# Kernel tuning notes

Measured on AMD Instinct MI355X. Metric: run time of the kernel, lower is better.

Reference implementation:

```python
import jax, jax.numpy as jnp
import numpy as np

B, T, C = 4, 2048, 1024
H, D = 16, 64  # num_heads, head_size


def setup_inputs() -> dict:
    key = jax.random.key(0)
    ks = jax.random.split(key, 5)
    s = 0.02
    x = jax.random.normal(ks[0], (B, T, C), dtype=jnp.float32)
    Wq = jax.random.normal(ks[1], (H, C, D), dtype=jnp.float32) * s
    Wk = jax.random.normal(ks[2], (H, C, D), dtype=jnp.float32) * s
    Wv = jax.random.normal(ks[3], (H, C, D), dtype=jnp.float32) * s
    Wp = jax.random.normal(ks[4], (C, H * D), dtype=jnp.float32) * s  # Linear(H*D, C) weight
    bp = jnp.zeros((C,), dtype=jnp.float32)
    return {"x": x, "Wq": Wq, "Wk": Wk, "Wv": Wv, "Wp": Wp, "bp": bp}


def reference(x, Wq, Wk, Wv, Wp, bp):
    # per-head projections (all heads batched): [B,T,C] x [H,C,D] -> [B,H,T,D]
    q = jnp.einsum('btc,hcd->bhtd', x, Wq)
    k = jnp.einsum('btc,hcd->bhtd', x, Wk)
    v = jnp.einsum('btc,hcd->bhtd', x, Wv)
    scale = 1.0 / jnp.sqrt(jnp.asarray(D, dtype=x.dtype))
    scores = jnp.einsum('bhtd,bhsd->bhts', q, k) * scale  # [B,H,T,T]
    causal = jnp.tril(jnp.ones((T, T), dtype=bool))
    scores = jnp.where(causal, scores, -jnp.inf)
    w = jax.nn.softmax(scores, axis=-1)
    out = jnp.einsum('bhts,bhsd->bhtd', w, v)  # [B,H,T,D]
    out = out.transpose(0, 2, 1, 3).reshape(B, T, H * D)  # concat heads
    return out @ Wp.T + bp  # projection (dropout is identity in eval)
```

## Files before the change

kernel.cpp:

```cpp
#include <hip/hip_runtime.h>
#include <stdint.h>


typedef unsigned short u16;
typedef __attribute__((ext_vector_type(8))) short    s16x8;
typedef __attribute__((ext_vector_type(4))) float    f32x4;
typedef __attribute__((ext_vector_type(2))) uint32_t u32x2;


__device__ __forceinline__ u16 f2b(float f) {
  union { float f; uint32_t u; } v; v.f = f;
  uint32_t r = v.u + 0x7FFFu + ((v.u >> 16) & 1u);
  return (u16)(r >> 16);
}

__device__ __forceinline__ uint32_t cvtpk(float a, float b) {
  uint32_t r;
  asm("v_cvt_pk_bf16_f32 %0, %1, %2" : "=v"(r) : "v"(a), "v"(b));
  return r;
}

__device__ __forceinline__ f32x4 mfma_bf16(s16x8 a, s16x8 b, f32x4 c) {
  asm("v_mfma_f32_16x16x32_bf16 %0, %1, %2, %0" : "+v"(c) : "v"(a), "v"(b));
  return c;
}

__device__ __forceinline__ void gload_lds16(const void* g, void* l) {
  __builtin_amdgcn_global_load_lds(
      (__attribute__((address_space(1))) void*)(uintptr_t)g,
      (__attribute__((address_space(3))) void*)(uint32_t)(uintptr_t)l,
      16, 0, 0);
}


__global__ void cvt_f32_bf16_kernel(const float* __restrict__ in, u16* __restrict__ out) {
  size_t i = (size_t)blockIdx.x * 256 + threadIdx.x;
  const f32x4* p = (const f32x4*)(in + i * 8);
  f32x4 a = p[0], b = p[1];
  s16x8 o;
  o[0]=(short)f2b(a[0]); o[1]=(short)f2b(a[1]); o[2]=(short)f2b(a[2]); o[3]=(short)f2b(a[3]);
  o[4]=(short)f2b(b[0]); o[5]=(short)f2b(b[1]); o[6]=(short)f2b(b[2]); o[7]=(short)f2b(b[3]);
  *(s16x8*)(out + i * 8) = o;
}

__global__ void cvt_wqkv_kernel(const float* __restrict__ Wq, const float* __restrict__ Wk,
                                const float* __restrict__ Wv, u16* __restrict__ out) {
  int idx = blockIdx.x * 256 + threadIdx.x;
  int sel = idx >> 20;
  int rem = idx & 1048575;
  int n = rem >> 10, c = rem & 1023;
  int h = n >> 6, d = n & 63;
  const float* W = (sel == 0) ? Wq : ((sel == 1) ? Wk : Wv);
  out[idx] = f2b(W[h * 65536 + c * 64 + d]);
}


template <bool OUT_F32, bool BIAS>
__global__ __launch_bounds__(256) void gemm_bt_kernel(
    const u16* __restrict__ A, const u16* __restrict__ B, void* __restrict__ Cout,
    const float* __restrict__ bias, int K, int ldc)
{
  __shared__ __attribute__((aligned(16))) u16 As[128 * 64];
  __shared__ __attribute__((aligned(16))) u16 Bs[128 * 64];

  const int tid  = threadIdx.x;
  const int lane = tid & 63;
  const int w    = tid >> 6;
  const int wm   = w >> 1, wn = w & 1;
  const int g    = lane >> 4;
  const int li   = lane & 15;
  const size_t bm = (size_t)blockIdx.x * 128;
  const size_t bn = (size_t)blockIdx.y * 128;

  f32x4 acc[4][4] = {};

  const int kIters = K >> 6;
  for (int kt = 0; kt < kIters; ++kt) {
    const int kb = kt * 64;
#pragma unroll
    for (int i = 0; i < 4; ++i) {
      int c = i * 256 + tid;
      int row = c >> 3, sl = c & 7;
      int ss = sl ^ (row & 7);
      gload_lds16(A + (bm + row) * K + kb + ss * 8, &As[c * 8]);
      gload_lds16(B + (bn + row) * K + kb + ss * 8, &Bs[c * 8]);
    }
    __syncthreads();
#pragma unroll
    for (int ks = 0; ks < 2; ++ks) {
      s16x8 af[4], bfr[4];
#pragma unroll
      for (int f = 0; f < 4; ++f) {
        int ra = wm * 64 + f * 16 + li;
        int sa = (ks * 4 + g) ^ (ra & 7);
        af[f] = *(const s16x8*)&As[ra * 64 + sa * 8];
        int rb = wn * 64 + f * 16 + li;
        int sb = (ks * 4 + g) ^ (rb & 7);
        bfr[f] = *(const s16x8*)&Bs[rb * 64 + sb * 8];
      }
#pragma unroll
      for (int mi = 0; mi < 4; ++mi)
#pragma unroll
        for (int ni = 0; ni < 4; ++ni)
          acc[mi][ni] = mfma_bf16(af[mi], bfr[ni], acc[mi][ni]);
    }
    __syncthreads();
  }

#pragma unroll
  for (int ni = 0; ni < 4; ++ni) {
    size_t col = bn + wn * 64 + ni * 16 + li;
    float bv = BIAS ? bias[col] : 0.f;
#pragma unroll
    for (int mi = 0; mi < 4; ++mi) {
#pragma unroll
      for (int r = 0; r < 4; ++r) {
        size_t row = bm + wm * 64 + mi * 16 + g * 4 + r;
        if constexpr (OUT_F32) ((float*)Cout)[row * ldc + col] = acc[mi][ni][r] + bv;
        else                   ((u16*)Cout)[row * ldc + col] = f2b(acc[mi][ni][r]);
      }
    }
  }
}


__global__ __launch_bounds__(256) void transpose_v_kernel(const u16* __restrict__ qkv,
                                                          u16* __restrict__ vT) {
  __shared__ __attribute__((aligned(16))) u16 ts[64][72];
  const int bh = blockIdx.y;
  const int b = bh >> 4, h = bh & 15;
  const int t0 = blockIdx.x * 64;
  const u16* src = qkv + (size_t)(b * 2048 + t0) * 3072 + 2048 + h * 64;
#pragma unroll
  for (int i = 0; i < 2; ++i) {
    int c = i * 256 + threadIdx.x;
    int row = c >> 3, sl = c & 7;
    *(s16x8*)&ts[row][sl * 8] = *(const s16x8*)&src[(size_t)row * 3072 + sl * 8];
  }
  __syncthreads();
  u16* dst = vT + (size_t)bh * 64 * 2048 + t0;
#pragma unroll
  for (int i = 0; i < 2; ++i) {
    int c = i * 256 + threadIdx.x;
    int drow = c >> 3, sl = c & 7;
    s16x8 o;
#pragma unroll
    for (int j = 0; j < 8; ++j) o[j] = (short)ts[sl * 8 + j][drow];
    *(s16x8*)&dst[(size_t)drow * 2048 + sl * 8] = o;
  }
}


__global__ __launch_bounds__(256) void attn_kernel(const u16* __restrict__ qkv,
                                                   const u16* __restrict__ vT,
                                                   u16* __restrict__ out) {
  __shared__ __attribute__((aligned(16))) u16 Ks[2][64 * 64];
  __shared__ __attribute__((aligned(16))) u16 Vs[2][64 * 64];
  __shared__ __attribute__((aligned(16))) u16 Ps[4][16 * 64];

  const int id  = blockIdx.x;
  const int xcd = id & 7;
  const int rr  = id >> 3;
  const int bh  = xcd * 8 + (rr & 7);
  const int p   = rr >> 3;

  const int b = bh >> 4, h = bh & 15;
  const int tid = threadIdx.x;
  const int lane = tid & 63;
  const int w = tid >> 6;
  const int g = lane >> 4, li = lane & 15;

  const int tA = 31 - p;
  const int nA = tA + 1;
  const int nTot = nA + p + 1;

  const u16* kbase = qkv + (size_t)(b * 2048) * 3072 + 1024 + h * 64;
  const u16* vtb   = vT + (size_t)bh * 64 * 2048;
  u16* pl = Ps[w];

  auto stage = [&](int buf, int j0) {
#pragma unroll
    for (int i = 0; i < 2; ++i) {
      int c = i * 256 + tid;
      int row = c >> 3, sl = c & 7, ss = sl ^ (row & 7);
      gload_lds16(kbase + (size_t)(j0 + row) * 3072 + ss * 8, &Ks[buf][c * 8]);
      gload_lds16(vtb + (size_t)row * 2048 + j0 + ss * 8, &Vs[buf][c * 8]);
    }
  };

  stage(0, 0);
  __syncthreads();

  s16x8 qf[2];
  f32x4 oacc[4];
  float mrow = -1e30f, lrow = 0.f;
  int wq0 = 0, qglob = 0;
  const float cexp = 0.18033688011112042f;

  for (int s = 0; s < nTot; ++s) {
    const int cur = s & 1;
    const bool inA = s < nA;
    const int t  = inA ? s : s - nA;
    const int qt = inA ? tA : p;
    const int j0 = t * 64;

    if (s + 1 < nTot) {
      int t1 = (s + 1 < nA) ? (s + 1) : (s + 1 - nA);
      stage(cur ^ 1, t1 * 64);
    }

    if (t == 0) {
      wq0 = qt * 64 + w * 16;
      qglob = wq0 + li;
      const u16* qbase = qkv + (size_t)(b * 2048 + qglob) * 3072 + h * 64;
#pragma unroll
      for (int kk = 0; kk < 2; ++kk)
        qf[kk] = *(const s16x8*)&qbase[kk * 32 + g * 8];
      mrow = -1e30f; lrow = 0.f;
#pragma unroll
      for (int fd = 0; fd < 4; ++fd) oacc[fd] = (f32x4)0.f;
    }

    const u16* ksb = Ks[cur];
    const u16* vsb = Vs[cur];

    f32x4 sfr[4] = {};
#pragma unroll
    for (int kk = 0; kk < 2; ++kk) {
      s16x8 kf[4];
#pragma unroll
      for (int fj = 0; fj < 4; ++fj) {
        int rk = fj * 16 + li;
        int ssl = (kk * 4 + g) ^ (rk & 7);
        kf[fj] = *(const s16x8*)&ksb[rk * 64 + ssl * 8];
      }
#pragma unroll
      for (int fj = 0; fj < 4; ++fj)
        sfr[fj] = mfma_bf16(kf[fj], qf[kk], sfr[fj]);
    }

    if (t == qt) {
#pragma unroll
      for (int fj = 0; fj < 4; ++fj)
#pragma unroll
        for (int r = 0; r < 4; ++r) {
          int jj = j0 + fj * 16 + g * 4 + r;
          if (jj > qglob) sfr[fj][r] = -1e30f;
        }
    }

    float mx = sfr[0][0];
#pragma unroll
    for (int fj = 0; fj < 4; ++fj)
#pragma unroll
      for (int r = 0; r < 4; ++r) mx = fmaxf(mx, sfr[fj][r]);
    mx = fmaxf(mx, __shfl_xor(mx, 16));
    mx = fmaxf(mx, __shfl_xor(mx, 32));

    bool need = (mx - mrow) * cexp > 8.0f;
    if (__any(need)) {
      float mnew = fmaxf(mrow, mx);
      float sc = exp2f((mrow - mnew) * cexp);
      mrow = mnew;
      lrow *= sc;
#pragma unroll
      for (int fd = 0; fd < 4; ++fd)
#pragma unroll
        for (int r = 0; r < 4; ++r) oacc[fd][r] *= sc;
    }

    float rs = 0.f;
    const int lsw = li & 14;
#pragma unroll
    for (int fj = 0; fj < 4; ++fj) {
      float p0 = exp2f((sfr[fj][0] - mrow) * cexp);
      float p1 = exp2f((sfr[fj][1] - mrow) * cexp);
      float p2 = exp2f((sfr[fj][2] - mrow) * cexp);
      float p3 = exp2f((sfr[fj][3] - mrow) * cexp);
      rs += (p0 + p1) + (p2 + p3);
      u32x2 wv = { cvtpk(p0, p1), cvtpk(p2, p3) };
      int phys = (4 * fj + g) ^ lsw;
      *(u32x2*)&pl[li * 64 + phys * 4] = wv;
    }
    rs += __shfl_xor(rs, 16);
    rs += __shfl_xor(rs, 32);
    lrow += rs;

#pragma unroll
    for (int kk = 0; kk < 2; ++kk) {
      int sr = (8 * kk + 2 * g) ^ lsw;
      s16x8 pf = *(const s16x8*)&pl[li * 64 + sr * 4];
      s16x8 vf[4];
#pragma unroll
      for (int fd = 0; fd < 4; ++fd) {
        int rv = fd * 16 + li;
        int ssl = (kk * 4 + g) ^ (rv & 7);
        vf[fd] = *(const s16x8*)&vsb[rv * 64 + ssl * 8];
      }
#pragma unroll
      for (int fd = 0; fd < 4; ++fd)
        oacc[fd] = mfma_bf16(vf[fd], pf, oacc[fd]);
    }

    if (t == qt) {
      float inv = 1.f / lrow;
      u16* ob = out + (size_t)(b * 2048 + qglob) * 1024 + h * 64;
#pragma unroll
      for (int fd = 0; fd < 4; ++fd) {
        u32x2 wv = { cvtpk(oacc[fd][0] * inv, oacc[fd][1] * inv),
                     cvtpk(oacc[fd][2] * inv, oacc[fd][3] * inv) };
        *(u32x2*)&ob[fd * 16 + g * 4] = wv;
      }
    }

    __syncthreads();
  }
}


extern "C" void kernel_launch(void* const* d_in, const int* in_sizes, int n_in,
                              void* d_out, int out_size, void* d_ws, size_t ws_size,
                              hipStream_t stream) {
  const float* x  = (const float*)d_in[0];
  const float* Wq = (const float*)d_in[1];
  const float* Wk = (const float*)d_in[2];
  const float* Wv = (const float*)d_in[3];
  const float* Wp = (const float*)d_in[4];
  const float* bp = (const float*)d_in[5];
  (void)in_sizes; (void)n_in; (void)out_size; (void)ws_size;

  char* ws = (char*)d_ws;
  u16* xb    = (u16*)(ws);
  u16* wqkvb = (u16*)(ws + 16777216);
  u16* wpb   = (u16*)(ws + 23068672);
  u16* qkv   = (u16*)(ws + 25165824);
  u16* vT    = (u16*)(ws + 75497472);
  u16* ao    = (u16*)(ws + 92274688);

  cvt_f32_bf16_kernel<<<4096, 256, 0, stream>>>(x, xb);
  cvt_wqkv_kernel<<<12288, 256, 0, stream>>>(Wq, Wk, Wv, wqkvb);
  cvt_f32_bf16_kernel<<<512, 256, 0, stream>>>(Wp, wpb);

  gemm_bt_kernel<false, false><<<dim3(64, 24), 256, 0, stream>>>(
      xb, wqkvb, (void*)qkv, nullptr, 1024, 3072);

  transpose_v_kernel<<<dim3(32, 64), 256, 0, stream>>>(qkv, vT);

  attn_kernel<<<1024, 256, 0, stream>>>(qkv, vT, ao);

  gemm_bt_kernel<true, true><<<dim3(64, 8), 256, 0, stream>>>(
      ao, wpb, d_out, bp, 1024, 1024);
}
```

Before: 182.2 us.

## Fuse V transpose into QKV GEMM epilogue and precompute attention LDS offsets

The QKV GEMM epilogue now writes V columns directly in transposed [B,H,D,T] layout with packed bf16 stores, removing the separate transpose kernel and its extra read/write pass over V. The attention kernel precomputes swizzled LDS fragment offsets and simplifies K/V staging address math. It also raises wave priority around the MFMA sections with s_setprio and adds a min-blocks launch bound to help occupancy. The transposed stores are strided 8-byte writes, which may be less coalesced than the old transpose kernel's output.

```diff
diff --git a/kernel.cpp b/kernel.cpp
--- a/kernel.cpp
+++ b/kernel.cpp
@@ -55,10 +55,10 @@
 }
 
 
-template <bool OUT_F32, bool BIAS>
+template <int MODE>
 __global__ __launch_bounds__(256) void gemm_bt_kernel(
     const u16* __restrict__ A, const u16* __restrict__ B, void* __restrict__ Cout,
-    const float* __restrict__ bias, int K, int ldc)
+    const float* __restrict__ bias, u16* __restrict__ vTout, int K, int ldc)
 {
   __shared__ __attribute__((aligned(16))) u16 As[128 * 64];
   __shared__ __attribute__((aligned(16))) u16 Bs[128 * 64];
@@ -107,53 +107,55 @@
     __syncthreads();
   }
 
-#pragma unroll
-  for (int ni = 0; ni < 4; ++ni) {
-    size_t col = bn + wn * 64 + ni * 16 + li;
-    float bv = BIAS ? bias[col] : 0.f;
-#pragma unroll
-    for (int mi = 0; mi < 4; ++mi) {
-#pragma unroll
-      for (int r = 0; r < 4; ++r) {
-        size_t row = bm + wm * 64 + mi * 16 + g * 4 + r;
-        if constexpr (OUT_F32) ((float*)Cout)[row * ldc + col] = acc[mi][ni][r] + bv;
-        else                   ((u16*)Cout)[row * ldc + col] = f2b(acc[mi][ni][r]);
+  if constexpr (MODE == 1) {
+#pragma unroll
+    for (int ni = 0; ni < 4; ++ni) {
+      size_t col = bn + wn * 64 + ni * 16 + li;
+      float bv = bias[col];
+#pragma unroll
+      for (int mi = 0; mi < 4; ++mi)
+#pragma unroll
+        for (int r = 0; r < 4; ++r) {
+          size_t row = bm + wm * 64 + mi * 16 + g * 4 + r;
+          ((float*)Cout)[row * ldc + col] = acc[mi][ni][r] + bv;
+        }
+    }
+  } else {
+    if (bn < 2048) {
+#pragma unroll
+      for (int ni = 0; ni < 4; ++ni) {
+        size_t col = bn + wn * 64 + ni * 16 + li;
+#pragma unroll
+        for (int mi = 0; mi < 4; ++mi)
+#pragma unroll
+          for (int r = 0; r < 4; ++r) {
+            size_t row = bm + wm * 64 + mi * 16 + g * 4 + r;
+            ((u16*)Cout)[row * ldc + col] = f2b(acc[mi][ni][r]);
+          }
       }
+    } else {
+      const int hb = (int)((bn - 2048) >> 6) + wn;
+      const int bb = (int)(bm >> 11);
+      const int t0b = ((int)bm & 2047) + wm * 64 + g * 4;
+      u16* vrow = vTout + (size_t)((bb * 16 + hb) * 64) * 2048;
+#pragma unroll
+      for (int ni = 0; ni < 4; ++ni) {
+        u16* vd_ = vrow + (size_t)(ni * 16 + li) * 2048;
+#pragma unroll
+        for (int mi = 0; mi < 4; ++mi) {
+          u32x2 wv = { cvtpk(acc[mi][ni][0], acc[mi][ni][1]),
+                       cvtpk(acc[mi][ni][2], acc[mi][ni][3]) };
+          *(u32x2*)&vd_[t0b + mi * 16] = wv;
+        }
+      }
     }
   }
 }
 
 
-__global__ __launch_bounds__(256) void transpose_v_kernel(const u16* __restrict__ qkv,
-                                                          u16* __restrict__ vT) {
-  __shared__ __attribute__((aligned(16))) u16 ts[64][72];
-  const int bh = blockIdx.y;
-  const int b = bh >> 4, h = bh & 15;
-  const int t0 = blockIdx.x * 64;
-  const u16* src = qkv + (size_t)(b * 2048 + t0) * 3072 + 2048 + h * 64;
-#pragma unroll
-  for (int i = 0; i < 2; ++i) {
-    int c = i * 256 + threadIdx.x;
-    int row = c >> 3, sl = c & 7;
-    *(s16x8*)&ts[row][sl * 8] = *(const s16x8*)&src[(size_t)row * 3072 + sl * 8];
-  }
-  __syncthreads();
-  u16* dst = vT + (size_t)bh * 64 * 2048 + t0;
-#pragma unroll
-  for (int i = 0; i < 2; ++i) {
-    int c = i * 256 + threadIdx.x;
-    int drow = c >> 3, sl = c & 7;
-    s16x8 o;
-#pragma unroll
-    for (int j = 0; j < 8; ++j) o[j] = (short)ts[sl * 8 + j][drow];
-    *(s16x8*)&dst[(size_t)drow * 2048 + sl * 8] = o;
-  }
-}
-
-
-__global__ __launch_bounds__(256) void attn_kernel(const u16* __restrict__ qkv,
-                                                   const u16* __restrict__ vT,
-                                                   u16* __restrict__ out) {
+__global__ __launch_bounds__(256, 4) void attn_kernel(const u16* __restrict__ qkv,
+                                                      const u16* __restrict__ vT,
+                                                      u16* __restrict__ out) {
   __shared__ __attribute__((aligned(16))) u16 Ks[2][64 * 64];
   __shared__ __attribute__((aligned(16))) u16 Vs[2][64 * 64];
   __shared__ __attribute__((aligned(16))) u16 Ps[4][16 * 64];
@@ -178,14 +180,37 @@
   const u16* vtb   = vT + (size_t)bh * 64 * 2048;
   u16* pl = Ps[w];
 
+  const int srow = tid >> 3;
+  const int ssl0 = (tid & 7) ^ (srow & 7);
+  const int kge0 = srow * 3072 + ssl0 * 8;
+  const int vge0 = srow * 2048 + ssl0 * 8;
+  u16* const kd0 = &Ks[0][tid * 8];
+  u16* const vd0 = &Vs[0][tid * 8];
+
+  int foff[2][4];
+#pragma unroll
+  for (int kk = 0; kk < 2; ++kk)
+#pragma unroll
+    for (int fj = 0; fj < 4; ++fj) {
+      int rk = fj * 16 + li;
+      foff[kk][fj] = rk * 64 + (((kk * 4 + g) ^ (rk & 7)) * 8);
+    }
+  const int lsw = li & 14;
+  int pwoff[4], proff[2];
+#pragma unroll
+  for (int fj = 0; fj < 4; ++fj) pwoff[fj] = li * 64 + (((4 * fj + g) ^ lsw) * 4);
+#pragma unroll
+  for (int kk = 0; kk < 2; ++kk) proff[kk] = li * 64 + (((8 * kk + 2 * g) ^ lsw) * 4);
+
   auto stage = [&](int buf, int j0) {
-#pragma unroll
-    for (int i = 0; i < 2; ++i) {
-      int c = i * 256 + tid;
-      int row = c >> 3, sl = c & 7, ss = sl ^ (row & 7);
-      gload_lds16(kbase + (size_t)(j0 + row) * 3072 + ss * 8, &Ks[buf][c * 8]);
-      gload_lds16(vtb + (size_t)row * 2048 + j0 + ss * 8, &Vs[buf][c * 8]);
-    }
+    const u16* kp = kbase + (size_t)j0 * 3072;
+    const u16* vp = vtb + j0;
+    u16* kd = kd0 + buf * 4096;
+    u16* vd = vd0 + buf * 4096;
+    gload_lds16(kp + kge0, kd);
+    gload_lds16(kp + kge0 + 32 * 3072, kd + 2048);
+    gload_lds16(vp + vge0, vd);
+    gload_lds16(vp + vge0 + 32 * 2048, vd + 2048);
   };
 
   stage(0, 0);
@@ -194,7 +219,7 @@
   s16x8 qf[2];
   f32x4 oacc[4];
   float mrow = -1e30f, lrow = 0.f;
-  int wq0 = 0, qglob = 0;
+  int qglob = 0;
   const float cexp = 0.18033688011112042f;
 
   for (int s = 0; s < nTot; ++s) {
@@ -210,8 +235,7 @@
     }
 
     if (t == 0) {
-      wq0 = qt * 64 + w * 16;
-      qglob = wq0 + li;
+      qglob = qt * 64 + w * 16 + li;
       const u16* qbase = qkv + (size_t)(b * 2048 + qglob) * 3072 + h * 64;
 #pragma unroll
       for (int kk = 0; kk < 2; ++kk)
@@ -221,23 +245,20 @@
       for (int fd = 0; fd < 4; ++fd) oacc[fd] = (f32x4)0.f;
     }
 
-    const u16* ksb = Ks[cur];
-    const u16* vsb = Vs[cur];
+    const u16* ksb = &Ks[0][0] + cur * 4096;
+    const u16* vsb = &Vs[0][0] + cur * 4096;
 
     f32x4 sfr[4] = {};
+    __builtin_amdgcn_s_setprio(1);
 #pragma unroll
     for (int kk = 0; kk < 2; ++kk) {
       s16x8 kf[4];
 #pragma unroll
-      for (int fj = 0; fj < 4; ++fj) {
-        int rk = fj * 16 + li;
-        int ssl = (kk * 4 + g) ^ (rk & 7);
-        kf[fj] = *(const s16x8*)&ksb[rk * 64 + ssl * 8];
-      }
-#pragma unroll
-      for (int fj = 0; fj < 4; ++fj)
-        sfr[fj] = mfma_bf16(kf[fj], qf[kk], sfr[fj]);
-    }
+      for (int fj = 0; fj < 4; ++fj) kf[fj] = *(const s16x8*)&ksb[foff[kk][fj]];
+#pragma unroll
+      for (int fj = 0; fj < 4; ++fj) sfr[fj] = mfma_bf16(kf[fj], qf[kk], sfr[fj]);
+    }
+    __builtin_amdgcn_s_setprio(0);
 
     if (t == qt) {
 #pragma unroll
@@ -270,7 +291,6 @@
     }
 
     float rs = 0.f;
-    const int lsw = li & 14;
 #pragma unroll
     for (int fj = 0; fj < 4; ++fj) {
       float p0 = exp2f((sfr[fj][0] - mrow) * cexp);
@@ -279,28 +299,23 @@
       float p3 = exp2f((sfr[fj][3] - mrow) * cexp);
       rs += (p0 + p1) + (p2 + p3);
       u32x2 wv = { cvtpk(p0, p1), cvtpk(p2, p3) };
-      int phys = (4 * fj + g) ^ lsw;
-      *(u32x2*)&pl[li * 64 + phys * 4] = wv;
+      *(u32x2*)&pl[pwoff[fj]] = wv;
     }
     rs += __shfl_xor(rs, 16);
     rs += __shfl_xor(rs, 32);
     lrow += rs;
 
+    __builtin_amdgcn_s_setprio(1);
 #pragma unroll
     for (int kk = 0; kk < 2; ++kk) {
-      int sr = (8 * kk + 2 * g) ^ lsw;
-      s16x8 pf = *(const s16x8*)&pl[li * 64 + sr * 4];
+      s16x8 pf = *(const s16x8*)&pl[proff[kk]];
       s16x8 vf[4];
 #pragma unroll
-      for (int fd = 0; fd < 4; ++fd) {
-        int rv = fd * 16 + li;
-        int ssl = (kk * 4 + g) ^ (rv & 7);
-        vf[fd] = *(const s16x8*)&vsb[rv * 64 + ssl * 8];
-      }
-#pragma unroll
-      for (int fd = 0; fd < 4; ++fd)
-        oacc[fd] = mfma_bf16(vf[fd], pf, oacc[fd]);
-    }
+      for (int fd = 0; fd < 4; ++fd) vf[fd] = *(const s16x8*)&vsb[foff[kk][fd]];
+#pragma unroll
+      for (int fd = 0; fd < 4; ++fd) oacc[fd] = mfma_bf16(vf[fd], pf, oacc[fd]);
+    }
+    __builtin_amdgcn_s_setprio(0);
 
     if (t == qt) {
       float inv = 1.f / lrow;
@@ -341,13 +356,11 @@
   cvt_wqkv_kernel<<<12288, 256, 0, stream>>>(Wq, Wk, Wv, wqkvb);
   cvt_f32_bf16_kernel<<<512, 256, 0, stream>>>(Wp, wpb);
 
-  gemm_bt_kernel<false, false><<<dim3(64, 24), 256, 0, stream>>>(
-      xb, wqkvb, (void*)qkv, nullptr, 1024, 3072);
-
-  transpose_v_kernel<<<dim3(32, 64), 256, 0, stream>>>(qkv, vT);
+  gemm_bt_kernel<2><<<dim3(64, 24), 256, 0, stream>>>(
+      xb, wqkvb, (void*)qkv, nullptr, vT, 1024, 3072);
 
   attn_kernel<<<1024, 256, 0, stream>>>(qkv, vT, ao);
 
-  gemm_bt_kernel<true, true><<<dim3(64, 8), 256, 0, stream>>>(
-      ao, wpb, d_out, bp, 1024, 1024);
-}
+  gemm_bt_kernel<1><<<dim3(64, 8), 256, 0, stream>>>(
+      ao, wpb, d_out, bp, nullptr, 1024, 1024);
+}
```

After: 175.7 us. 1.04x faster.
